# Kernel optimization log

Measured on AMD Instinct MI355X. Metric: run time of the kernel, lower is better.

Reference implementation:

```python
import jax, jax.numpy as jnp
import numpy as np

Q = 8192      # num query tokens
S = 32768     # num support points
E = 131072    # num edges (query<-support neighbor pairs)
D = 256       # token_dim
H = 8         # num_heads
HD = D // H   # head_dim = 32
GEO = 128     # geo mlp_hidden = geo_dim
FFN = 2 * D   # ffn hidden
STAT_IN = 12  # 4 stats * 3 coords
EPS_LN = 1e-5


def gelu(x):
    return jax.nn.gelu(x, approximate=False)  # torch nn.GELU default (erf)


def layernorm(x, g, b):
    m = jnp.mean(x, axis=-1, keepdims=True)
    v = jnp.mean((x - m) ** 2, axis=-1, keepdims=True)
    return (x - m) * jax.lax.rsqrt(v + EPS_LN) * g + b


def setup_inputs() -> dict:
    key = jax.random.key(0)
    ks = jax.random.split(key, 16)
    w = lambda k, shp: jax.random.normal(k, shp, jnp.float32) * 0.02
    return {
        "query_tokens": jax.random.normal(ks[0], (Q, D), jnp.float32),
        "query_pos": jax.random.normal(ks[1], (Q, 3), jnp.float32),
        "support_feats": jax.random.normal(ks[2], (S, D), jnp.float32),
        "support_pos": jax.random.normal(ks[3], (S, 3), jnp.float32),
        "Wq": w(ks[4], (D, D)), "Wk": w(ks[5], (D, D)), "Wv": w(ks[6], (D, D)),
        "Wg": w(ks[7], (GEO, D)),
        "Wo": w(ks[8], (D, D)), "bo": jnp.zeros((D,), jnp.float32),
        "log_tau": jnp.array(0.0, jnp.float32),
        "ln1_g": jnp.ones((D,), jnp.float32), "ln1_b": jnp.zeros((D,), jnp.float32),
        "ln2_g": jnp.ones((D,), jnp.float32), "ln2_b": jnp.zeros((D,), jnp.float32),
        "Wf1": w(ks[9], (D, FFN)), "bf1": jnp.zeros((FFN,), jnp.float32),
        "Wf2": w(ks[10], (FFN, D)), "bf2": jnp.zeros((D,), jnp.float32),
        "Gw1": w(ks[11], (STAT_IN, GEO)), "Gb1": jnp.zeros((GEO,), jnp.float32),
        "Gw2": w(ks[12], (GEO, GEO)), "Gb2": jnp.zeros((GEO,), jnp.float32),
        "q_idx": jnp.sort(jax.random.randint(ks[13], (E,), 0, Q)),
        "s_idx": jax.random.randint(ks[14], (E,), 0, S),
        "num_queries": Q,
    }


def geo_stats(rel, q_idx, num_q):
    # rel: [E,3] relative positions; segmented mean/std/min/max -> [num_q, 12]
    ones = jnp.ones((rel.shape[0], 1), rel.dtype)
    cnt = jnp.maximum(jax.ops.segment_sum(ones, q_idx, num_q), 1.0)  # [Q,1]
    mean = jax.ops.segment_sum(rel, q_idx, num_q) / cnt
    var = jax.ops.segment_sum((rel - mean[q_idx]) ** 2, q_idx, num_q) / cnt
    std = jnp.sqrt(var)
    # torch inits min/max with +/-inf then clamps to [-100,100]; jax segment
    # min/max init with dtype extremes -> same result after clip
    mn = jnp.clip(jax.ops.segment_min(rel, q_idx, num_q), -100.0, 100.0)
    mx = jnp.clip(jax.ops.segment_max(rel, q_idx, num_q), -100.0, 100.0)
    return jnp.concatenate([mean, std, mn, mx], axis=-1)


def reference(query_tokens, query_pos, support_feats, support_pos,
              Wq, Wk, Wv, Wg, Wo, bo, log_tau,
              ln1_g, ln1_b, ln2_g, ln2_b,
              Wf1, bf1, Wf2, bf2, Gw1, Gb1, Gw2, Gb2,
              q_idx, s_idx, num_queries):
    num_q = num_queries
    # ---- statistical geo embedding ----
    rel = support_pos[s_idx] - query_pos[q_idx]                 # [E,3]
    raw = geo_stats(rel, q_idx, num_q)                          # [Q,12]
    geo = gelu(gelu(raw @ Gw1 + Gb1) @ Gw2 + Gb2)               # [Q,GEO]

    # ---- AGNO cross attention (pre-norm) ----
    qt = layernorm(query_tokens, ln1_g, ln1_b)
    Qf = qt @ Wq                                                # [Q,D]
    Kf = support_feats @ Wk                                     # [S,D]
    Vf = support_feats @ Wv                                     # [S,D]
    Gf = geo @ Wg                                               # [Q,D]
    qh = Qf[q_idx].reshape(E, H, HD)
    kh = Kf[s_idx].reshape(E, H, HD)
    vh = Vf[s_idx].reshape(E, H, HD)
    gh = Gf[q_idx].reshape(E, H, HD)
    tau = jnp.exp(log_tau)
    scores = jnp.sum(qh * kh, axis=-1) / (jnp.sqrt(jnp.float32(HD)) * tau)  # [E,H]
    # torch scores_max starts at 0 -> max(0, segment max)
    smax = jnp.maximum(jax.ops.segment_max(scores, q_idx, num_q), 0.0)
    ex = jnp.exp(scores - smax[q_idx])
    ssum = jax.ops.segment_sum(ex, q_idx, num_q)
    alpha = ex / jnp.maximum(ssum[q_idx], 1e-8)                 # [E,H]
    weighted = alpha[..., None] * (vh + gh)                     # [E,H,HD]
    out = jax.ops.segment_sum(weighted, q_idx, num_q)           # [Q,H,HD]
    attn = out.reshape(num_q, D) @ Wo + bo

    # ---- residual + FFN ----
    x = query_tokens + attn
    x = x + gelu(layernorm(x, ln2_g, ln2_b) @ Wf1 + bf1) @ Wf2 + bf2
    return x
```

## Files before the change

### kernel.cpp

```cpp
#include <hip/hip_runtime.h>
#include <math.h>

#define QN 8192
#define SN 32768
#define EN 131072
#define DN 256
#define HN 8
#define HDN 32
#define GEON 128
#define FFNN 512

typedef __attribute__((ext_vector_type(8))) short bf16x8;
typedef __attribute__((ext_vector_type(8))) unsigned short u16x8;
typedef __attribute__((ext_vector_type(4))) unsigned short u16x4;
typedef __attribute__((ext_vector_type(4))) float f32x4;

__device__ __forceinline__ unsigned short f2b(float f) {
  union { float f; unsigned u; } v; v.f = f;
  unsigned u = v.u;
  u += 0x7fffu + ((u >> 16) & 1u);
  return (unsigned short)(u >> 16);
}
__device__ __forceinline__ float b2f(unsigned short h) {
  union { unsigned u; float f; } v; v.u = ((unsigned)h) << 16; return v.f;
}
__device__ __forceinline__ float gelu_f(float x) {
  return 0.5f * x * (1.0f + erff(x * 0.70710678118654752440f));
}

__global__ __launch_bounds__(256) void transpose_weights(
    const float* Wq, const float* Wk, const float* Wv, const float* Wg,
    const float* Wo, const float* Wf1, const float* Wf2,
    unsigned short* WqT, unsigned short* WkvT, unsigned short* WgT,
    unsigned short* WoT, unsigned short* Wf1T, unsigned short* Wf2T) {
  int b = blockIdx.x;
  const float* src; unsigned short* dst; int K, N, tile;
  if (b < 16)       { src = Wq;  dst = WqT;          K = 256; N = 256; tile = b; }
  else if (b < 32)  { src = Wk;  dst = WkvT;         K = 256; N = 256; tile = b - 16; }
  else if (b < 48)  { src = Wv;  dst = WkvT + 65536; K = 256; N = 256; tile = b - 32; }
  else if (b < 56)  { src = Wg;  dst = WgT;          K = 128; N = 256; tile = b - 48; }
  else if (b < 72)  { src = Wo;  dst = WoT;          K = 256; N = 256; tile = b - 56; }
  else if (b < 104) { src = Wf1; dst = Wf1T;         K = 256; N = 512; tile = b - 72; }
  else              { src = Wf2; dst = Wf2T;         K = 512; N = 256; tile = b - 104; }
  int ktiles = K >> 6;
  int k0 = (tile % ktiles) * 64, n0 = (tile / ktiles) * 64;
  __shared__ float ts[64][65];
  int t = threadIdx.x;
  int c4 = (t & 15) * 4;
  int r = t >> 4;
#pragma unroll
  for (int p = 0; p < 4; ++p) {
    int row = p * 16 + r;
    float4 v = *(const float4*)(src + (size_t)(k0 + row) * N + n0 + c4);
    ts[row][c4 + 0] = v.x; ts[row][c4 + 1] = v.y;
    ts[row][c4 + 2] = v.z; ts[row][c4 + 3] = v.w;
  }
  __syncthreads();
#pragma unroll
  for (int p = 0; p < 4; ++p) {
    int n = p * 16 + r;
    ushort4 o;
    o.x = f2b(ts[c4 + 0][n]); o.y = f2b(ts[c4 + 1][n]);
    o.z = f2b(ts[c4 + 2][n]); o.w = f2b(ts[c4 + 3][n]);
    *(ushort4*)(dst + (size_t)(n0 + n) * K + k0 + c4) = o;
  }
}

__global__ __launch_bounds__(256) void seg_offsets(const int* q_idx, int* offs) {
  int i = blockIdx.x * 256 + threadIdx.x;
  if (i > QN) return;
  int lo = 0, hi = EN;
  while (lo < hi) {
    int mid = (lo + hi) >> 1;
    if (q_idx[mid] < i) lo = mid + 1; else hi = mid;
  }
  offs[i] = lo;
}

__global__ __launch_bounds__(256) void geo_stats_kernel(
    const float* qpos, const float* spos, const int* offs, const int* s_idx, float* raw) {
  int q = blockIdx.x * 64 + (threadIdx.x >> 2);
  int sub = threadIdx.x & 3;
  int e0 = offs[q], e1 = offs[q + 1];
  float qx = qpos[q * 3 + 0], qy = qpos[q * 3 + 1], qz = qpos[q * 3 + 2];
  float cnt = 0.f, sx = 0.f, sy = 0.f, sz = 0.f, sxx = 0.f, syy = 0.f, szz = 0.f;
  float mnx = 1e30f, mny = 1e30f, mnz = 1e30f, mxx = -1e30f, mxy = -1e30f, mxz = -1e30f;
  for (int e = e0 + sub; e < e1; e += 4) {
    int s = s_idx[e];
    float rx = spos[s * 3 + 0] - qx;
    float ry = spos[s * 3 + 1] - qy;
    float rz = spos[s * 3 + 2] - qz;
    cnt += 1.f;
    sx += rx; sy += ry; sz += rz;
    sxx += rx * rx; syy += ry * ry; szz += rz * rz;
    mnx = fminf(mnx, rx); mny = fminf(mny, ry); mnz = fminf(mnz, rz);
    mxx = fmaxf(mxx, rx); mxy = fmaxf(mxy, ry); mxz = fmaxf(mxz, rz);
  }
#pragma unroll
  for (int msk = 1; msk <= 2; msk <<= 1) {
    cnt += __shfl_xor(cnt, msk);
    sx += __shfl_xor(sx, msk); sy += __shfl_xor(sy, msk); sz += __shfl_xor(sz, msk);
    sxx += __shfl_xor(sxx, msk); syy += __shfl_xor(syy, msk); szz += __shfl_xor(szz, msk);
    mnx = fminf(mnx, __shfl_xor(mnx, msk));
    mny = fminf(mny, __shfl_xor(mny, msk));
    mnz = fminf(mnz, __shfl_xor(mnz, msk));
    mxx = fmaxf(mxx, __shfl_xor(mxx, msk));
    mxy = fmaxf(mxy, __shfl_xor(mxy, msk));
    mxz = fmaxf(mxz, __shfl_xor(mxz, msk));
  }
  if (sub == 0) {
    float c = fmaxf(cnt, 1.f);
    float mx_ = sx / c, my_ = sy / c, mz_ = sz / c;
    float vx = fmaxf(sxx / c - mx_ * mx_, 0.f);
    float vy = fmaxf(syy / c - my_ * my_, 0.f);
    float vz = fmaxf(szz / c - mz_ * mz_, 0.f);
    float* r = raw + (size_t)q * 12;
    r[0] = mx_; r[1] = my_; r[2] = mz_;
    r[3] = sqrtf(vx); r[4] = sqrtf(vy); r[5] = sqrtf(vz);
    r[6] = fminf(fmaxf(mnx, -100.f), 100.f);
    r[7] = fminf(fmaxf(mny, -100.f), 100.f);
    r[8] = fminf(fmaxf(mnz, -100.f), 100.f);
    r[9] = fminf(fmaxf(mxx, -100.f), 100.f);
    r[10] = fminf(fmaxf(mxy, -100.f), 100.f);
    r[11] = fminf(fmaxf(mxz, -100.f), 100.f);
  }
}

__global__ __launch_bounds__(128) void geo_mlp_kernel(
    const float* raw, const float* Gw1, const float* Gb1,
    const float* Gw2, const float* Gb2, unsigned short* geo_b) {
  int qb = blockIdx.x * 8;
  int j = threadIdx.x;
  __shared__ float rs[8][12];
  __shared__ float h1[8][128];
  if (j < 96) rs[j / 12][j % 12] = raw[(size_t)(qb + j / 12) * 12 + (j % 12)];
  __syncthreads();
  float b1 = Gb1[j];
  float acc[8];
#pragma unroll
  for (int qq = 0; qq < 8; ++qq) acc[qq] = b1;
  for (int i = 0; i < 12; ++i) {
    float w = Gw1[i * GEON + j];
#pragma unroll
    for (int qq = 0; qq < 8; ++qq) acc[qq] += rs[qq][i] * w;
  }
#pragma unroll
  for (int qq = 0; qq < 8; ++qq) h1[qq][j] = gelu_f(acc[qq]);
  __syncthreads();
  float b2 = Gb2[j];
  float acc2[8];
#pragma unroll
  for (int qq = 0; qq < 8; ++qq) acc2[qq] = b2;
  for (int k = 0; k < 128; ++k) {
    float w = Gw2[k * GEON + j];
#pragma unroll
    for (int qq = 0; qq < 8; ++qq) acc2[qq] += h1[qq][k] * w;
  }
#pragma unroll
  for (int qq = 0; qq < 8; ++qq)
    geo_b[(size_t)(qb + qq) * GEON + j] = f2b(gelu_f(acc2[qq]));
}

__global__ __launch_bounds__(256) void ln_kernel(
    const float* x, const float* g, const float* b, unsigned short* out) {
  int row = blockIdx.x * 4 + (threadIdx.x >> 6);
  int lane = threadIdx.x & 63;
  const float* xr = x + (size_t)row * DN;
  float4 v = *(const float4*)(xr + lane * 4);
  float s = v.x + v.y + v.z + v.w;
  float ss = v.x * v.x + v.y * v.y + v.z * v.z + v.w * v.w;
#pragma unroll
  for (int msk = 1; msk <= 32; msk <<= 1) {
    s += __shfl_xor(s, msk);
    ss += __shfl_xor(ss, msk);
  }
  float mean = s * (1.f / 256.f);
  float var = ss * (1.f / 256.f) - mean * mean;
  float rs = 1.0f / sqrtf(var + 1e-5f);
  float4 gg = *(const float4*)(g + lane * 4);
  float4 bb = *(const float4*)(b + lane * 4);
  unsigned short* o = out + (size_t)row * DN + lane * 4;
  o[0] = f2b((v.x - mean) * rs * gg.x + bb.x);
  o[1] = f2b((v.y - mean) * rs * gg.y + bb.y);
  o[2] = f2b((v.z - mean) * rs * gg.z + bb.z);
  o[3] = f2b((v.w - mean) * rs * gg.w + bb.w);
}

__device__ __forceinline__ u16x8* lds_g(unsigned short* base, int row, int col) {
  int g = (col >> 3) ^ (row & 7);
  return reinterpret_cast<u16x8*>(base + row * 256 + g * 8);
}
__global__ __launch_bounds__(256) void kv_gemm(
    const float* A, const unsigned short* BT, unsigned short* KVb) {
  __shared__ unsigned short As[64 * 256];
  __shared__ unsigned short Bs[32 * 256];
  int t = threadIdx.x;
  int bm = blockIdx.x * 64;
  int w = t >> 6, lane = t & 63;
  int quad = lane >> 4, l16 = lane & 15;
  int wr = w >> 1, wc = w & 1;
  int srow = t >> 2, sub = t & 3;
  {
    const float* Ag = A + (size_t)(bm + srow) * 256 + sub * 64;
#pragma unroll
    for (int i = 0; i < 8; ++i) {
      float4 f0 = *(const float4*)(Ag + i * 8);
      float4 f1 = *(const float4*)(Ag + i * 8 + 4);
      u16x8 u;
      u[0] = f2b(f0.x); u[1] = f2b(f0.y); u[2] = f2b(f0.z); u[3] = f2b(f0.w);
      u[4] = f2b(f1.x); u[5] = f2b(f1.y); u[6] = f2b(f1.z); u[7] = f2b(f1.w);
      *lds_g(As, srow, sub * 64 + i * 8) = u;
    }
  }
  int brow = t >> 3, bsub = t & 7;
  for (int ct = 0; ct < 16; ++ct) {
    {
      const unsigned short* Bg = BT + (size_t)(ct * 32 + brow) * 256 + bsub * 32;
#pragma unroll
      for (int i = 0; i < 4; ++i)
        *lds_g(Bs, brow, bsub * 32 + i * 8) = *reinterpret_cast<const u16x8*>(Bg + i * 8);
    }
    __syncthreads();
    f32x4 acc[2];
    acc[0] = (f32x4){0.f, 0.f, 0.f, 0.f};
    acc[1] = (f32x4){0.f, 0.f, 0.f, 0.f};
#pragma unroll
    for (int k = 0; k < 8; ++k) {
      bf16x8 a0 = *reinterpret_cast<bf16x8*>(lds_g(As, wr * 32 + l16, k * 32 + quad * 8));
      bf16x8 a1 = *reinterpret_cast<bf16x8*>(lds_g(As, wr * 32 + 16 + l16, k * 32 + quad * 8));
      bf16x8 b0 = *reinterpret_cast<bf16x8*>(lds_g(Bs, wc * 16 + l16, k * 32 + quad * 8));
      acc[0] = __builtin_amdgcn_mfma_f32_16x16x32_bf16(a0, b0, acc[0], 0, 0, 0);
      acc[1] = __builtin_amdgcn_mfma_f32_16x16x32_bf16(a1, b0, acc[1], 0, 0, 0);
    }
#pragma unroll
    for (int i = 0; i < 2; ++i)
#pragma unroll
      for (int r = 0; r < 4; ++r) {
        int rw = bm + wr * 32 + i * 16 + quad * 4 + r;
        int col = ct * 32 + wc * 16 + l16;
        KVb[(size_t)rw * 512 + col] = f2b(acc[i][r]);
      }
    __syncthreads();
  }
}

template <bool A_FP32, bool COLGRID, bool HAS_BIAS, bool DO_GELU, bool HAS_RESID, bool STORE_F32>
__global__ __launch_bounds__(256) void gemm64(
    const void* Ap, const unsigned short* BT, int M, int N, int K,
    const float* bias, const float* resid, float* outF, unsigned short* outB) {
  __shared__ unsigned short As[64][40];
  __shared__ unsigned short Bs[64][40];
  int t = threadIdx.x;
  int bm = (COLGRID ? blockIdx.x : blockIdx.y) * 64;
  int bn = (COLGRID ? blockIdx.y : blockIdx.x) * 64;
  int w = t >> 6, lane = t & 63;
  int wr = w >> 1, wc = w & 1;
  int quad = lane >> 4, l16 = lane & 15;
  int row = t >> 2, chunk = t & 3;

  f32x4 acc[2][2];
#pragma unroll
  for (int i = 0; i < 2; ++i)
#pragma unroll
    for (int j = 0; j < 2; ++j) acc[i][j] = (f32x4){0.f, 0.f, 0.f, 0.f};

  for (int k0 = 0; k0 < K; k0 += 32) {
    if (A_FP32) {
      const float* Ag = (const float*)Ap + (size_t)(bm + row) * K + k0 + chunk * 8;
      float4 f0 = *(const float4*)Ag;
      float4 f1 = *(const float4*)(Ag + 4);
      u16x8 u;
      u[0] = f2b(f0.x); u[1] = f2b(f0.y); u[2] = f2b(f0.z); u[3] = f2b(f0.w);
      u[4] = f2b(f1.x); u[5] = f2b(f1.y); u[6] = f2b(f1.z); u[7] = f2b(f1.w);
      *reinterpret_cast<u16x8*>(&As[row][chunk * 8]) = u;
    } else {
      const unsigned short* Ag = (const unsigned short*)Ap + (size_t)(bm + row) * K + k0 + chunk * 8;
      *reinterpret_cast<u16x8*>(&As[row][chunk * 8]) = *reinterpret_cast<const u16x8*>(Ag);
    }
    {
      const unsigned short* Bg = BT + (size_t)(bn + row) * K + k0 + chunk * 8;
      *reinterpret_cast<u16x8*>(&Bs[row][chunk * 8]) = *reinterpret_cast<const u16x8*>(Bg);
    }
    __syncthreads();
    bf16x8 a0 = *reinterpret_cast<const bf16x8*>(&As[wr * 32 + l16][quad * 8]);
    bf16x8 a1 = *reinterpret_cast<const bf16x8*>(&As[wr * 32 + 16 + l16][quad * 8]);
    bf16x8 b0 = *reinterpret_cast<const bf16x8*>(&Bs[wc * 32 + l16][quad * 8]);
    bf16x8 b1 = *reinterpret_cast<const bf16x8*>(&Bs[wc * 32 + 16 + l16][quad * 8]);
    acc[0][0] = __builtin_amdgcn_mfma_f32_16x16x32_bf16(a0, b0, acc[0][0], 0, 0, 0);
    acc[0][1] = __builtin_amdgcn_mfma_f32_16x16x32_bf16(a0, b1, acc[0][1], 0, 0, 0);
    acc[1][0] = __builtin_amdgcn_mfma_f32_16x16x32_bf16(a1, b0, acc[1][0], 0, 0, 0);
    acc[1][1] = __builtin_amdgcn_mfma_f32_16x16x32_bf16(a1, b1, acc[1][1], 0, 0, 0);
    __syncthreads();
  }

#pragma unroll
  for (int i = 0; i < 2; ++i)
#pragma unroll
    for (int j = 0; j < 2; ++j) {
      int col = bn + wc * 32 + j * 16 + l16;
      float bv = HAS_BIAS ? bias[col] : 0.f;
#pragma unroll
      for (int r = 0; r < 4; ++r) {
        int rw = bm + wr * 32 + i * 16 + quad * 4 + r;
        float v = acc[i][j][r] + bv;
        if (DO_GELU) v = gelu_f(v);
        if (HAS_RESID) v += resid[(size_t)rw * N + col];
        if (STORE_F32) outF[(size_t)rw * N + col] = v;
        else outB[(size_t)rw * N + col] = f2b(v);
      }
    }
}

__global__ __launch_bounds__(256) void attn_edge_kernel(
    const unsigned short* Qb, const unsigned short* Gfb, const unsigned short* KVb,
    const int* s_idx, const int* offs, const float* log_tau, unsigned short* attn_b) {
  int q = blockIdx.x * 4 + (threadIdx.x >> 6);
  int lane = threadIdx.x & 63;
  int half = lane >> 5;
  int sl = lane & 31;
  int d0 = sl * 8;
  int e0 = offs[q], e1 = offs[q + 1];
  float invs = expf(-log_tau[0]) * 0.17677669529663687f;
  u16x8 qu = *(const u16x8*)(Qb + (size_t)q * DN + d0);
  u16x8 gu = *(const u16x8*)(Gfb + (size_t)q * DN + d0);
  float qf[8], gf[8];
#pragma unroll
  for (int j = 0; j < 8; ++j) { qf[j] = b2f(qu[j]) * invs; gf[j] = b2f(gu[j]); }
  const float NEG = -1e30f;
  float m = -INFINITY, l = 0.f;
  float a[8];
#pragma unroll
  for (int j = 0; j < 8; ++j) a[j] = 0.f;
  for (int e = e0; e < e1; e += 2) {
    int ee = e + half;
    bool valid = ee < e1;
    int s = s_idx[valid ? ee : (e1 - 1)];
    const unsigned short* kr = KVb + (size_t)s * 512 + d0;
    u16x8 ku = *(const u16x8*)kr;
    u16x8 vu = *(const u16x8*)(kr + 256);
    float p = 0.f;
#pragma unroll
    for (int j = 0; j < 8; ++j) p += qf[j] * b2f(ku[j]);
    p += __shfl_xor(p, 1);
    p += __shfl_xor(p, 2);
    if (!valid) p = -INFINITY;
    float mnew = fmaxf(m, p);
    float sc = (m > NEG) ? __expf(m - mnew) : 0.f;
    float we = valid ? __expf(p - mnew) : 0.f;
    l = l * sc + we;
#pragma unroll
    for (int j = 0; j < 8; ++j) a[j] = a[j] * sc + we * (b2f(vu[j]) + gf[j]);
    m = mnew;
  }
  float om = __shfl_xor(m, 32);
  float ol = __shfl_xor(l, 32);
  float M2 = fmaxf(m, om);
  float ws = (m > NEG) ? __expf(m - M2) : 0.f;
  float wo = (om > NEG) ? __expf(om - M2) : 0.f;
  l = l * ws + ol * wo;
#pragma unroll
  for (int j = 0; j < 8; ++j) {
    float oa = __shfl_xor(a[j], 32);
    a[j] = a[j] * ws + oa * wo;
  }
  float M = fmaxf(M2, 0.f);
  float em = (M2 > NEG) ? __expf(M2 - M) : 0.f;
  float denom = fmaxf(l * em, 1e-8f);
  float f = em / denom;
  if (half == 0) {
    u16x8 o;
#pragma unroll
    for (int j = 0; j < 8; ++j) o[j] = f2b(a[j] * f);
    *(u16x8*)(attn_b + (size_t)q * DN + d0) = o;
  }
}

extern "C" void kernel_launch(void* const* d_in, const int* in_sizes, int n_in,
                              void* d_out, int out_size, void* d_ws, size_t ws_size,
                              hipStream_t stream) {
  const float* query_tokens  = (const float*)d_in[0];
  const float* query_pos     = (const float*)d_in[1];
  const float* support_feats = (const float*)d_in[2];
  const float* support_pos   = (const float*)d_in[3];
  const float* Wq  = (const float*)d_in[4];
  const float* Wk  = (const float*)d_in[5];
  const float* Wv  = (const float*)d_in[6];
  const float* Wg  = (const float*)d_in[7];
  const float* Wo  = (const float*)d_in[8];
  const float* bo  = (const float*)d_in[9];
  const float* log_tau = (const float*)d_in[10];
  const float* ln1_g = (const float*)d_in[11];
  const float* ln1_b = (const float*)d_in[12];
  const float* ln2_g = (const float*)d_in[13];
  const float* ln2_b = (const float*)d_in[14];
  const float* Wf1 = (const float*)d_in[15];
  const float* bf1 = (const float*)d_in[16];
  const float* Wf2 = (const float*)d_in[17];
  const float* bf2 = (const float*)d_in[18];
  const float* Gw1 = (const float*)d_in[19];
  const float* Gb1 = (const float*)d_in[20];
  const float* Gw2 = (const float*)d_in[21];
  const float* Gb2 = (const float*)d_in[22];
  const int* q_idx = (const int*)d_in[23];
  const int* s_idx = (const int*)d_in[24];
  float* out = (float*)d_out;

  char* ws = (char*)d_ws;
  size_t off = 0;
  auto alloc = [&](size_t bytes) -> void* {
    void* p = ws + off;
    off = (off + bytes + 255) & ~(size_t)255;
    return p;
  };
  unsigned short* WqT  = (unsigned short*)alloc(65536 * 2);
  unsigned short* WkvT = (unsigned short*)alloc(131072 * 2);
  unsigned short* WgT  = (unsigned short*)alloc(32768 * 2);
  unsigned short* WoT  = (unsigned short*)alloc(65536 * 2);
  unsigned short* Wf1T = (unsigned short*)alloc(131072 * 2);
  unsigned short* Wf2T = (unsigned short*)alloc(131072 * 2);
  int* offs            = (int*)alloc((QN + 1) * 4);
  float* raw           = (float*)alloc((size_t)QN * 12 * 4);
  unsigned short* geo_b = (unsigned short*)alloc((size_t)QN * GEON * 2);
  unsigned short* qt_b  = (unsigned short*)alloc((size_t)QN * DN * 2);
  unsigned short* Qb    = (unsigned short*)alloc((size_t)QN * DN * 2);
  unsigned short* Gf_b  = (unsigned short*)alloc((size_t)QN * DN * 2);
  unsigned short* KVb   = (unsigned short*)alloc((size_t)SN * 512 * 2);
  unsigned short* attn_b = (unsigned short*)alloc((size_t)QN * DN * 2);
  float* x1             = (float*)alloc((size_t)QN * DN * 4);
  unsigned short* z_b   = (unsigned short*)alloc((size_t)QN * DN * 2);
  unsigned short* h_b   = (unsigned short*)alloc((size_t)QN * FFNN * 2);

  transpose_weights<<<136, 256, 0, stream>>>(Wq, Wk, Wv, Wg, Wo, Wf1, Wf2,
                                             WqT, WkvT, WgT, WoT, Wf1T, Wf2T);
  seg_offsets<<<33, 256, 0, stream>>>(q_idx, offs);
  geo_stats_kernel<<<QN / 64, 256, 0, stream>>>(query_pos, support_pos, offs, s_idx, raw);
  geo_mlp_kernel<<<QN / 8, 128, 0, stream>>>(raw, Gw1, Gb1, Gw2, Gb2, geo_b);
  ln_kernel<<<QN / 4, 256, 0, stream>>>(query_tokens, ln1_g, ln1_b, qt_b);
  kv_gemm<<<SN / 64, 256, 0, stream>>>(support_feats, WkvT, KVb);
  gemm64<false, true, false, false, false, false><<<dim3(QN / 64, DN / 64), 256, 0, stream>>>(
      qt_b, WqT, QN, DN, 256, nullptr, nullptr, nullptr, Qb);
  gemm64<false, true, false, false, false, false><<<dim3(QN / 64, DN / 64), 256, 0, stream>>>(
      geo_b, WgT, QN, DN, 128, nullptr, nullptr, nullptr, Gf_b);
  attn_edge_kernel<<<QN / 4, 256, 0, stream>>>(Qb, Gf_b, KVb, s_idx, offs, log_tau, attn_b);
  gemm64<false, true, true, false, true, true><<<dim3(QN / 64, DN / 64), 256, 0, stream>>>(
      attn_b, WoT, QN, DN, 256, bo, query_tokens, x1, nullptr);
  ln_kernel<<<QN / 4, 256, 0, stream>>>(x1, ln2_g, ln2_b, z_b);
  gemm64<false, true, true, true, false, false><<<dim3(QN / 64, FFNN / 64), 256, 0, stream>>>(
      z_b, Wf1T, QN, FFNN, 256, bf1, nullptr, nullptr, h_b);
  gemm64<false, true, true, false, true, true><<<dim3(QN / 64, DN / 64), 256, 0, stream>>>(
      h_b, Wf2T, QN, DN, 512, bf2, x1, out, nullptr);

  (void)in_sizes; (void)n_in; (void)out_size; (void)ws_size;
}
```

Baseline: 252.9 us.

## Fuse LayerNorms into full-K panel GEMMs and prefetch KV weight tiles

Removes both standalone LayerNorm kernels by computing row statistics inside a new single-panel GEMM that loads the whole K extent into LDS, and moves the Q, G, Wo and Wf1 GEMMs onto this panel kernel. kv_gemm now prefetches the next B tile into registers while the current tile is used in MFMAs. The attention kernel stops adding gf to every edge's value and instead adds gf scaled by the normalized softmax mass once at output. These changes cut kernel launches, intermediate bf16 round trips and per-edge ALU work. In exchange the panel kernel uses large LDS buffers, and the LN fusion recomputes the row statistics in every N-column block.

```diff
diff --git a/kernel.cpp b/kernel.cpp
--- a/kernel.cpp
+++ b/kernel.cpp
@@ -26,6 +26,12 @@
 }
 __device__ __forceinline__ float gelu_f(float x) {
   return 0.5f * x * (1.0f + erff(x * 0.70710678118654752440f));
+}
+
+template <int KT>
+__device__ __forceinline__ u16x8* lds_gk(unsigned short* base, int row, int col) {
+  int g = (col >> 3) ^ (row & 7);
+  return reinterpret_cast<u16x8*>(base + row * KT + g * 8);
 }
 
 __global__ __launch_bounds__(256) void transpose_weights(
@@ -161,35 +167,6 @@
     geo_b[(size_t)(qb + qq) * GEON + j] = f2b(gelu_f(acc2[qq]));
 }
 
-__global__ __launch_bounds__(256) void ln_kernel(
-    const float* x, const float* g, const float* b, unsigned short* out) {
-  int row = blockIdx.x * 4 + (threadIdx.x >> 6);
-  int lane = threadIdx.x & 63;
-  const float* xr = x + (size_t)row * DN;
-  float4 v = *(const float4*)(xr + lane * 4);
-  float s = v.x + v.y + v.z + v.w;
-  float ss = v.x * v.x + v.y * v.y + v.z * v.z + v.w * v.w;
-#pragma unroll
-  for (int msk = 1; msk <= 32; msk <<= 1) {
-    s += __shfl_xor(s, msk);
-    ss += __shfl_xor(ss, msk);
-  }
-  float mean = s * (1.f / 256.f);
-  float var = ss * (1.f / 256.f) - mean * mean;
-  float rs = 1.0f / sqrtf(var + 1e-5f);
-  float4 gg = *(const float4*)(g + lane * 4);
-  float4 bb = *(const float4*)(b + lane * 4);
-  unsigned short* o = out + (size_t)row * DN + lane * 4;
-  o[0] = f2b((v.x - mean) * rs * gg.x + bb.x);
-  o[1] = f2b((v.y - mean) * rs * gg.y + bb.y);
-  o[2] = f2b((v.z - mean) * rs * gg.z + bb.z);
-  o[3] = f2b((v.w - mean) * rs * gg.w + bb.w);
-}
-
-__device__ __forceinline__ u16x8* lds_g(unsigned short* base, int row, int col) {
-  int g = (col >> 3) ^ (row & 7);
-  return reinterpret_cast<u16x8*>(base + row * 256 + g * 8);
-}
 __global__ __launch_bounds__(256) void kv_gemm(
     const float* A, const unsigned short* BT, unsigned short* KVb) {
   __shared__ unsigned short As[64 * 256];
@@ -209,26 +186,34 @@
       u16x8 u;
       u[0] = f2b(f0.x); u[1] = f2b(f0.y); u[2] = f2b(f0.z); u[3] = f2b(f0.w);
       u[4] = f2b(f1.x); u[5] = f2b(f1.y); u[6] = f2b(f1.z); u[7] = f2b(f1.w);
-      *lds_g(As, srow, sub * 64 + i * 8) = u;
+      *lds_gk<256>(As, srow, sub * 64 + i * 8) = u;
     }
   }
   int brow = t >> 3, bsub = t & 7;
+  u16x8 pre[4];
+  {
+    const unsigned short* Bg = BT + (size_t)brow * 256 + bsub * 32;
+#pragma unroll
+    for (int i = 0; i < 4; ++i) pre[i] = *reinterpret_cast<const u16x8*>(Bg + i * 8);
+  }
   for (int ct = 0; ct < 16; ++ct) {
-    {
-      const unsigned short* Bg = BT + (size_t)(ct * 32 + brow) * 256 + bsub * 32;
-#pragma unroll
-      for (int i = 0; i < 4; ++i)
-        *lds_g(Bs, brow, bsub * 32 + i * 8) = *reinterpret_cast<const u16x8*>(Bg + i * 8);
-    }
+#pragma unroll
+    for (int i = 0; i < 4; ++i)
+      *lds_gk<256>(Bs, brow, bsub * 32 + i * 8) = pre[i];
     __syncthreads();
+    if (ct < 15) {
+      const unsigned short* Bg = BT + (size_t)((ct + 1) * 32 + brow) * 256 + bsub * 32;
+#pragma unroll
+      for (int i = 0; i < 4; ++i) pre[i] = *reinterpret_cast<const u16x8*>(Bg + i * 8);
+    }
     f32x4 acc[2];
     acc[0] = (f32x4){0.f, 0.f, 0.f, 0.f};
     acc[1] = (f32x4){0.f, 0.f, 0.f, 0.f};
 #pragma unroll
     for (int k = 0; k < 8; ++k) {
-      bf16x8 a0 = *reinterpret_cast<bf16x8*>(lds_g(As, wr * 32 + l16, k * 32 + quad * 8));
-      bf16x8 a1 = *reinterpret_cast<bf16x8*>(lds_g(As, wr * 32 + 16 + l16, k * 32 + quad * 8));
-      bf16x8 b0 = *reinterpret_cast<bf16x8*>(lds_g(Bs, wc * 16 + l16, k * 32 + quad * 8));
+      bf16x8 a0 = *reinterpret_cast<bf16x8*>(lds_gk<256>(As, wr * 32 + l16, k * 32 + quad * 8));
+      bf16x8 a1 = *reinterpret_cast<bf16x8*>(lds_gk<256>(As, wr * 32 + 16 + l16, k * 32 + quad * 8));
+      bf16x8 b0 = *reinterpret_cast<bf16x8*>(lds_gk<256>(Bs, wc * 16 + l16, k * 32 + quad * 8));
       acc[0] = __builtin_amdgcn_mfma_f32_16x16x32_bf16(a0, b0, acc[0], 0, 0, 0);
       acc[1] = __builtin_amdgcn_mfma_f32_16x16x32_bf16(a1, b0, acc[1], 0, 0, 0);
     }
@@ -242,6 +227,106 @@
       }
     __syncthreads();
   }
+}
+
+template <int KT, int AMODE, bool HAS_BIAS, bool DO_GELU, bool HAS_RESID, bool STORE_F32>
+__global__ __launch_bounds__(256) void gemm_panel(
+    const void* Ap, const unsigned short* BT, int N,
+    const float* lng, const float* lnb,
+    const float* bias, const float* resid, float* outF, unsigned short* outB) {
+  __shared__ unsigned short As[64 * KT];
+  __shared__ unsigned short Bs[64 * KT];
+  int t = threadIdx.x;
+  int bm = blockIdx.x * 64, bn = blockIdx.y * 64;
+  int row = t >> 2, sub = t & 3;
+  constexpr int CH = KT / 4;
+
+  if constexpr (AMODE == 1) {
+    static_assert(KT == 256, "LN fusion assumes D=256 rows");
+    const float* Ag = (const float*)Ap + (size_t)(bm + row) * 256 + sub * 64;
+    float va[64];
+    float s = 0.f, ss = 0.f;
+#pragma unroll
+    for (int i = 0; i < 16; ++i) {
+      float4 v = *(const float4*)(Ag + i * 4);
+      va[i * 4 + 0] = v.x; va[i * 4 + 1] = v.y;
+      va[i * 4 + 2] = v.z; va[i * 4 + 3] = v.w;
+      s += v.x + v.y + v.z + v.w;
+      ss += v.x * v.x + v.y * v.y + v.z * v.z + v.w * v.w;
+    }
+    s += __shfl_xor(s, 1);  s += __shfl_xor(s, 2);
+    ss += __shfl_xor(ss, 1); ss += __shfl_xor(ss, 2);
+    float mean = s * (1.f / 256.f);
+    float var = ss * (1.f / 256.f) - mean * mean;
+    float rstd = 1.0f / sqrtf(var + 1e-5f);
+#pragma unroll
+    for (int i = 0; i < 8; ++i) {
+      int c0 = sub * 64 + i * 8;
+      float4 g0 = *(const float4*)(lng + c0);
+      float4 g1 = *(const float4*)(lng + c0 + 4);
+      float4 b0 = *(const float4*)(lnb + c0);
+      float4 b1 = *(const float4*)(lnb + c0 + 4);
+      u16x8 u;
+      u[0] = f2b((va[i * 8 + 0] - mean) * rstd * g0.x + b0.x);
+      u[1] = f2b((va[i * 8 + 1] - mean) * rstd * g0.y + b0.y);
+      u[2] = f2b((va[i * 8 + 2] - mean) * rstd * g0.z + b0.z);
+      u[3] = f2b((va[i * 8 + 3] - mean) * rstd * g0.w + b0.w);
+      u[4] = f2b((va[i * 8 + 4] - mean) * rstd * g1.x + b1.x);
+      u[5] = f2b((va[i * 8 + 5] - mean) * rstd * g1.y + b1.y);
+      u[6] = f2b((va[i * 8 + 6] - mean) * rstd * g1.z + b1.z);
+      u[7] = f2b((va[i * 8 + 7] - mean) * rstd * g1.w + b1.w);
+      *lds_gk<256>(As, row, c0) = u;
+    }
+  } else {
+    const unsigned short* Ag = (const unsigned short*)Ap + (size_t)(bm + row) * KT + sub * CH;
+#pragma unroll
+    for (int i = 0; i < CH / 8; ++i)
+      *lds_gk<KT>(As, row, sub * CH + i * 8) = *reinterpret_cast<const u16x8*>(Ag + i * 8);
+  }
+  {
+    const unsigned short* Bg = BT + (size_t)(bn + row) * KT + sub * CH;
+#pragma unroll
+    for (int i = 0; i < CH / 8; ++i)
+      *lds_gk<KT>(Bs, row, sub * CH + i * 8) = *reinterpret_cast<const u16x8*>(Bg + i * 8);
+  }
+  __syncthreads();
+
+  int w = t >> 6, lane = t & 63;
+  int wr = w >> 1, wc = w & 1;
+  int quad = lane >> 4, l16 = lane & 15;
+  f32x4 acc[2][2];
+#pragma unroll
+  for (int i = 0; i < 2; ++i)
+#pragma unroll
+    for (int j = 0; j < 2; ++j) acc[i][j] = (f32x4){0.f, 0.f, 0.f, 0.f};
+#pragma unroll
+  for (int k = 0; k < KT / 32; ++k) {
+    bf16x8 a0 = *reinterpret_cast<bf16x8*>(lds_gk<KT>(As, wr * 32 + l16, k * 32 + quad * 8));
+    bf16x8 a1 = *reinterpret_cast<bf16x8*>(lds_gk<KT>(As, wr * 32 + 16 + l16, k * 32 + quad * 8));
+    bf16x8 b0 = *reinterpret_cast<bf16x8*>(lds_gk<KT>(Bs, wc * 32 + l16, k * 32 + quad * 8));
+    bf16x8 b1 = *reinterpret_cast<bf16x8*>(lds_gk<KT>(Bs, wc * 32 + 16 + l16, k * 32 + quad * 8));
+    acc[0][0] = __builtin_amdgcn_mfma_f32_16x16x32_bf16(a0, b0, acc[0][0], 0, 0, 0);
+    acc[0][1] = __builtin_amdgcn_mfma_f32_16x16x32_bf16(a0, b1, acc[0][1], 0, 0, 0);
+    acc[1][0] = __builtin_amdgcn_mfma_f32_16x16x32_bf16(a1, b0, acc[1][0], 0, 0, 0);
+    acc[1][1] = __builtin_amdgcn_mfma_f32_16x16x32_bf16(a1, b1, acc[1][1], 0, 0, 0);
+  }
+
+#pragma unroll
+  for (int i = 0; i < 2; ++i)
+#pragma unroll
+    for (int j = 0; j < 2; ++j) {
+      int col = bn + wc * 32 + j * 16 + l16;
+      float bv = HAS_BIAS ? bias[col] : 0.f;
+#pragma unroll
+      for (int r = 0; r < 4; ++r) {
+        int rw = bm + wr * 32 + i * 16 + quad * 4 + r;
+        float v = acc[i][j][r] + bv;
+        if (DO_GELU) v = gelu_f(v);
+        if (HAS_RESID) v += resid[(size_t)rw * N + col];
+        if (STORE_F32) outF[(size_t)rw * N + col] = v;
+        else outB[(size_t)rw * N + col] = f2b(v);
+      }
+    }
 }
 
 template <bool A_FP32, bool COLGRID, bool HAS_BIAS, bool DO_GELU, bool HAS_RESID, bool STORE_F32>
@@ -349,7 +434,7 @@
     float we = valid ? __expf(p - mnew) : 0.f;
     l = l * sc + we;
 #pragma unroll
-    for (int j = 0; j < 8; ++j) a[j] = a[j] * sc + we * (b2f(vu[j]) + gf[j]);
+    for (int j = 0; j < 8; ++j) a[j] = a[j] * sc + we * b2f(vu[j]);
     m = mnew;
   }
   float om = __shfl_xor(m, 32);
@@ -367,10 +452,11 @@
   float em = (M2 > NEG) ? __expf(M2 - M) : 0.f;
   float denom = fmaxf(l * em, 1e-8f);
   float f = em / denom;
+  float sa = l * f;
   if (half == 0) {
     u16x8 o;
 #pragma unroll
-    for (int j = 0; j < 8; ++j) o[j] = f2b(a[j] * f);
+    for (int j = 0; j < 8; ++j) o[j] = f2b(a[j] * f + gf[j] * sa);
     *(u16x8*)(attn_b + (size_t)q * DN + d0) = o;
   }
 }
@@ -421,13 +507,11 @@
   int* offs            = (int*)alloc((QN + 1) * 4);
   float* raw           = (float*)alloc((size_t)QN * 12 * 4);
   unsigned short* geo_b = (unsigned short*)alloc((size_t)QN * GEON * 2);
-  unsigned short* qt_b  = (unsigned short*)alloc((size_t)QN * DN * 2);
   unsigned short* Qb    = (unsigned short*)alloc((size_t)QN * DN * 2);
   unsigned short* Gf_b  = (unsigned short*)alloc((size_t)QN * DN * 2);
   unsigned short* KVb   = (unsigned short*)alloc((size_t)SN * 512 * 2);
   unsigned short* attn_b = (unsigned short*)alloc((size_t)QN * DN * 2);
   float* x1             = (float*)alloc((size_t)QN * DN * 4);
-  unsigned short* z_b   = (unsigned short*)alloc((size_t)QN * DN * 2);
   unsigned short* h_b   = (unsigned short*)alloc((size_t)QN * FFNN * 2);
 
   transpose_weights<<<136, 256, 0, stream>>>(Wq, Wk, Wv, Wg, Wo, Wf1, Wf2,
@@ -435,18 +519,16 @@
   seg_offsets<<<33, 256, 0, stream>>>(q_idx, offs);
   geo_stats_kernel<<<QN / 64, 256, 0, stream>>>(query_pos, support_pos, offs, s_idx, raw);
   geo_mlp_kernel<<<QN / 8, 128, 0, stream>>>(raw, Gw1, Gb1, Gw2, Gb2, geo_b);
-  ln_kernel<<<QN / 4, 256, 0, stream>>>(query_tokens, ln1_g, ln1_b, qt_b);
   kv_gemm<<<SN / 64, 256, 0, stream>>>(support_feats, WkvT, KVb);
-  gemm64<false, true, false, false, false, false><<<dim3(QN / 64, DN / 64), 256, 0, stream>>>(
-      qt_b, WqT, QN, DN, 256, nullptr, nullptr, nullptr, Qb);
-  gemm64<false, true, false, false, false, false><<<dim3(QN / 64, DN / 64), 256, 0, stream>>>(
-      geo_b, WgT, QN, DN, 128, nullptr, nullptr, nullptr, Gf_b);
+  gemm_panel<256, 1, false, false, false, false><<<dim3(QN / 64, 4), 256, 0, stream>>>(
+      query_tokens, WqT, DN, ln1_g, ln1_b, nullptr, nullptr, nullptr, Qb);
+  gemm_panel<128, 0, false, false, false, false><<<dim3(QN / 64, 4), 256, 0, stream>>>(
+      geo_b, WgT, DN, nullptr, nullptr, nullptr, nullptr, nullptr, Gf_b);
   attn_edge_kernel<<<QN / 4, 256, 0, stream>>>(Qb, Gf_b, KVb, s_idx, offs, log_tau, attn_b);
-  gemm64<false, true, true, false, true, true><<<dim3(QN / 64, DN / 64), 256, 0, stream>>>(
-      attn_b, WoT, QN, DN, 256, bo, query_tokens, x1, nullptr);
-  ln_kernel<<<QN / 4, 256, 0, stream>>>(x1, ln2_g, ln2_b, z_b);
-  gemm64<false, true, true, true, false, false><<<dim3(QN / 64, FFNN / 64), 256, 0, stream>>>(
-      z_b, Wf1T, QN, FFNN, 256, bf1, nullptr, nullptr, h_b);
+  gemm_panel<256, 0, true, false, true, true><<<dim3(QN / 64, 4), 256, 0, stream>>>(
+      attn_b, WoT, DN, nullptr, nullptr, bo, query_tokens, x1, nullptr);
+  gemm_panel<256, 1, true, true, false, false><<<dim3(QN / 64, 8), 256, 0, stream>>>(
+      x1, Wf1T, FFNN, ln2_g, ln2_b, bf1, nullptr, nullptr, h_b);
   gemm64<false, true, true, false, true, true><<<dim3(QN / 64, DN / 64), 256, 0, stream>>>(
       h_b, Wf2T, QN, DN, 512, bf2, x1, out, nullptr);
 
```

After: 276.0 us. 1.09x slower.

## Prefetch GEMM tiles into registers and process four edges per wave in attention

Applied to the files above, without the earlier changes.

Both the kv_gemm and generic gemm64 kernels now load the next K/B tile from global memory into registers before the MFMA loop runs on the current tile. The goal is to overlap global-load latency with compute. The attention edge kernel now has each wave process four edges at a time with 16-wide dims per lane instead of two edges with 8-wide dims, which halves the shuffle-reduction depth per dot product. The geometric term is also pulled out of the per-edge accumulate and added once at the end, scaled by the normalized weight sum. These changes raise register pressure and make the final merge across slots more complex.

```diff
diff --git a/kernel.cpp b/kernel.cpp
--- a/kernel.cpp
+++ b/kernel.cpp
@@ -26,6 +26,12 @@
 }
 __device__ __forceinline__ float gelu_f(float x) {
   return 0.5f * x * (1.0f + erff(x * 0.70710678118654752440f));
+}
+
+template <int KT>
+__device__ __forceinline__ u16x8* lds_gk(unsigned short* base, int row, int col) {
+  int g = (col >> 3) ^ (row & 7);
+  return reinterpret_cast<u16x8*>(base + row * KT + g * 8);
 }
 
 __global__ __launch_bounds__(256) void transpose_weights(
@@ -186,10 +192,6 @@
   o[3] = f2b((v.w - mean) * rs * gg.w + bb.w);
 }
 
-__device__ __forceinline__ u16x8* lds_g(unsigned short* base, int row, int col) {
-  int g = (col >> 3) ^ (row & 7);
-  return reinterpret_cast<u16x8*>(base + row * 256 + g * 8);
-}
 __global__ __launch_bounds__(256) void kv_gemm(
     const float* A, const unsigned short* BT, unsigned short* KVb) {
   __shared__ unsigned short As[64 * 256];
@@ -209,26 +211,34 @@
       u16x8 u;
       u[0] = f2b(f0.x); u[1] = f2b(f0.y); u[2] = f2b(f0.z); u[3] = f2b(f0.w);
       u[4] = f2b(f1.x); u[5] = f2b(f1.y); u[6] = f2b(f1.z); u[7] = f2b(f1.w);
-      *lds_g(As, srow, sub * 64 + i * 8) = u;
+      *lds_gk<256>(As, srow, sub * 64 + i * 8) = u;
     }
   }
   int brow = t >> 3, bsub = t & 7;
+  u16x8 pre[4];
+  {
+    const unsigned short* Bg = BT + (size_t)brow * 256 + bsub * 32;
+#pragma unroll
+    for (int i = 0; i < 4; ++i) pre[i] = *reinterpret_cast<const u16x8*>(Bg + i * 8);
+  }
   for (int ct = 0; ct < 16; ++ct) {
-    {
-      const unsigned short* Bg = BT + (size_t)(ct * 32 + brow) * 256 + bsub * 32;
-#pragma unroll
-      for (int i = 0; i < 4; ++i)
-        *lds_g(Bs, brow, bsub * 32 + i * 8) = *reinterpret_cast<const u16x8*>(Bg + i * 8);
-    }
+#pragma unroll
+    for (int i = 0; i < 4; ++i)
+      *lds_gk<256>(Bs, brow, bsub * 32 + i * 8) = pre[i];
     __syncthreads();
+    if (ct < 15) {
+      const unsigned short* Bg = BT + (size_t)((ct + 1) * 32 + brow) * 256 + bsub * 32;
+#pragma unroll
+      for (int i = 0; i < 4; ++i) pre[i] = *reinterpret_cast<const u16x8*>(Bg + i * 8);
+    }
     f32x4 acc[2];
     acc[0] = (f32x4){0.f, 0.f, 0.f, 0.f};
     acc[1] = (f32x4){0.f, 0.f, 0.f, 0.f};
 #pragma unroll
     for (int k = 0; k < 8; ++k) {
-      bf16x8 a0 = *reinterpret_cast<bf16x8*>(lds_g(As, wr * 32 + l16, k * 32 + quad * 8));
-      bf16x8 a1 = *reinterpret_cast<bf16x8*>(lds_g(As, wr * 32 + 16 + l16, k * 32 + quad * 8));
-      bf16x8 b0 = *reinterpret_cast<bf16x8*>(lds_g(Bs, wc * 16 + l16, k * 32 + quad * 8));
+      bf16x8 a0 = *reinterpret_cast<bf16x8*>(lds_gk<256>(As, wr * 32 + l16, k * 32 + quad * 8));
+      bf16x8 a1 = *reinterpret_cast<bf16x8*>(lds_gk<256>(As, wr * 32 + 16 + l16, k * 32 + quad * 8));
+      bf16x8 b0 = *reinterpret_cast<bf16x8*>(lds_gk<256>(Bs, wc * 16 + l16, k * 32 + quad * 8));
       acc[0] = __builtin_amdgcn_mfma_f32_16x16x32_bf16(a0, b0, acc[0], 0, 0, 0);
       acc[1] = __builtin_amdgcn_mfma_f32_16x16x32_bf16(a1, b0, acc[1], 0, 0, 0);
     }
@@ -258,6 +268,16 @@
   int quad = lane >> 4, l16 = lane & 15;
   int row = t >> 2, chunk = t & 3;
 
+  const float* AgF = (const float*)Ap + (size_t)(bm + row) * K + chunk * 8;
+  const unsigned short* AgB = (const unsigned short*)Ap + (size_t)(bm + row) * K + chunk * 8;
+  const unsigned short* Bg = BT + (size_t)(bn + row) * K + chunk * 8;
+
+  float4 pf0, pf1;
+  u16x8 pa, pb;
+  if (A_FP32) { pf0 = *(const float4*)AgF; pf1 = *(const float4*)(AgF + 4); }
+  else        { pa = *(const u16x8*)AgB; }
+  pb = *(const u16x8*)Bg;
+
   f32x4 acc[2][2];
 #pragma unroll
   for (int i = 0; i < 2; ++i)
@@ -265,23 +285,21 @@
     for (int j = 0; j < 2; ++j) acc[i][j] = (f32x4){0.f, 0.f, 0.f, 0.f};
 
   for (int k0 = 0; k0 < K; k0 += 32) {
+    u16x8 ua;
     if (A_FP32) {
-      const float* Ag = (const float*)Ap + (size_t)(bm + row) * K + k0 + chunk * 8;
-      float4 f0 = *(const float4*)Ag;
-      float4 f1 = *(const float4*)(Ag + 4);
-      u16x8 u;
-      u[0] = f2b(f0.x); u[1] = f2b(f0.y); u[2] = f2b(f0.z); u[3] = f2b(f0.w);
-      u[4] = f2b(f1.x); u[5] = f2b(f1.y); u[6] = f2b(f1.z); u[7] = f2b(f1.w);
-      *reinterpret_cast<u16x8*>(&As[row][chunk * 8]) = u;
+      ua[0] = f2b(pf0.x); ua[1] = f2b(pf0.y); ua[2] = f2b(pf0.z); ua[3] = f2b(pf0.w);
+      ua[4] = f2b(pf1.x); ua[5] = f2b(pf1.y); ua[6] = f2b(pf1.z); ua[7] = f2b(pf1.w);
     } else {
-      const unsigned short* Ag = (const unsigned short*)Ap + (size_t)(bm + row) * K + k0 + chunk * 8;
-      *reinterpret_cast<u16x8*>(&As[row][chunk * 8]) = *reinterpret_cast<const u16x8*>(Ag);
-    }
-    {
-      const unsigned short* Bg = BT + (size_t)(bn + row) * K + k0 + chunk * 8;
-      *reinterpret_cast<u16x8*>(&Bs[row][chunk * 8]) = *reinterpret_cast<const u16x8*>(Bg);
-    }
+      ua = pa;
+    }
+    *reinterpret_cast<u16x8*>(&As[row][chunk * 8]) = ua;
+    *reinterpret_cast<u16x8*>(&Bs[row][chunk * 8]) = pb;
     __syncthreads();
+    if (k0 + 32 < K) {
+      if (A_FP32) { pf0 = *(const float4*)(AgF + k0 + 32); pf1 = *(const float4*)(AgF + k0 + 36); }
+      else        { pa = *(const u16x8*)(AgB + k0 + 32); }
+      pb = *(const u16x8*)(Bg + k0 + 32);
+    }
     bf16x8 a0 = *reinterpret_cast<const bf16x8*>(&As[wr * 32 + l16][quad * 8]);
     bf16x8 a1 = *reinterpret_cast<const bf16x8*>(&As[wr * 32 + 16 + l16][quad * 8]);
     bf16x8 b0 = *reinterpret_cast<const bf16x8*>(&Bs[wc * 32 + l16][quad * 8]);
@@ -316,62 +334,83 @@
     const int* s_idx, const int* offs, const float* log_tau, unsigned short* attn_b) {
   int q = blockIdx.x * 4 + (threadIdx.x >> 6);
   int lane = threadIdx.x & 63;
-  int half = lane >> 5;
-  int sl = lane & 31;
-  int d0 = sl * 8;
+  int slot = lane >> 4;
+  int sl = lane & 15;
+  int d0 = sl * 16;
   int e0 = offs[q], e1 = offs[q + 1];
   float invs = expf(-log_tau[0]) * 0.17677669529663687f;
-  u16x8 qu = *(const u16x8*)(Qb + (size_t)q * DN + d0);
-  u16x8 gu = *(const u16x8*)(Gfb + (size_t)q * DN + d0);
-  float qf[8], gf[8];
-#pragma unroll
-  for (int j = 0; j < 8; ++j) { qf[j] = b2f(qu[j]) * invs; gf[j] = b2f(gu[j]); }
+  u16x8 qu0 = *(const u16x8*)(Qb + (size_t)q * DN + d0);
+  u16x8 qu1 = *(const u16x8*)(Qb + (size_t)q * DN + d0 + 8);
+  u16x8 gu0 = *(const u16x8*)(Gfb + (size_t)q * DN + d0);
+  u16x8 gu1 = *(const u16x8*)(Gfb + (size_t)q * DN + d0 + 8);
+  float qf[16], gf[16];
+#pragma unroll
+  for (int j = 0; j < 8; ++j) {
+    qf[j] = b2f(qu0[j]) * invs; qf[j + 8] = b2f(qu1[j]) * invs;
+    gf[j] = b2f(gu0[j]);        gf[j + 8] = b2f(gu1[j]);
+  }
   const float NEG = -1e30f;
   float m = -INFINITY, l = 0.f;
-  float a[8];
-#pragma unroll
-  for (int j = 0; j < 8; ++j) a[j] = 0.f;
-  for (int e = e0; e < e1; e += 2) {
-    int ee = e + half;
+  float a[16];
+#pragma unroll
+  for (int j = 0; j < 16; ++j) a[j] = 0.f;
+  for (int e = e0; e < e1; e += 4) {
+    int ee = e + slot;
     bool valid = ee < e1;
     int s = s_idx[valid ? ee : (e1 - 1)];
     const unsigned short* kr = KVb + (size_t)s * 512 + d0;
-    u16x8 ku = *(const u16x8*)kr;
-    u16x8 vu = *(const u16x8*)(kr + 256);
+    u16x8 ku0 = *(const u16x8*)kr;
+    u16x8 ku1 = *(const u16x8*)(kr + 8);
+    u16x8 vu0 = *(const u16x8*)(kr + 256);
+    u16x8 vu1 = *(const u16x8*)(kr + 264);
     float p = 0.f;
 #pragma unroll
-    for (int j = 0; j < 8; ++j) p += qf[j] * b2f(ku[j]);
+    for (int j = 0; j < 8; ++j) {
+      p += qf[j] * b2f(ku0[j]);
+      p += qf[j + 8] * b2f(ku1[j]);
+    }
     p += __shfl_xor(p, 1);
-    p += __shfl_xor(p, 2);
     if (!valid) p = -INFINITY;
     float mnew = fmaxf(m, p);
     float sc = (m > NEG) ? __expf(m - mnew) : 0.f;
     float we = valid ? __expf(p - mnew) : 0.f;
     l = l * sc + we;
 #pragma unroll
-    for (int j = 0; j < 8; ++j) a[j] = a[j] * sc + we * (b2f(vu[j]) + gf[j]);
+    for (int j = 0; j < 8; ++j) {
+      a[j] = a[j] * sc + we * b2f(vu0[j]);
+      a[j + 8] = a[j + 8] * sc + we * b2f(vu1[j]);
+    }
     m = mnew;
   }
-  float om = __shfl_xor(m, 32);
-  float ol = __shfl_xor(l, 32);
-  float M2 = fmaxf(m, om);
-  float ws = (m > NEG) ? __expf(m - M2) : 0.f;
-  float wo = (om > NEG) ? __expf(om - M2) : 0.f;
-  l = l * ws + ol * wo;
-#pragma unroll
-  for (int j = 0; j < 8; ++j) {
-    float oa = __shfl_xor(a[j], 32);
-    a[j] = a[j] * ws + oa * wo;
-  }
-  float M = fmaxf(M2, 0.f);
-  float em = (M2 > NEG) ? __expf(M2 - M) : 0.f;
+#pragma unroll
+  for (int msk = 16; msk <= 32; msk <<= 1) {
+    float om = __shfl_xor(m, msk);
+    float ol = __shfl_xor(l, msk);
+    float M2 = fmaxf(m, om);
+    float ws = (m > NEG) ? __expf(m - M2) : 0.f;
+    float wo = (om > NEG) ? __expf(om - M2) : 0.f;
+    l = l * ws + ol * wo;
+#pragma unroll
+    for (int j = 0; j < 16; ++j) {
+      float oa = __shfl_xor(a[j], msk);
+      a[j] = a[j] * ws + oa * wo;
+    }
+    m = M2;
+  }
+  float M = fmaxf(m, 0.f);
+  float em = (m > NEG) ? __expf(m - M) : 0.f;
   float denom = fmaxf(l * em, 1e-8f);
   float f = em / denom;
-  if (half == 0) {
-    u16x8 o;
-#pragma unroll
-    for (int j = 0; j < 8; ++j) o[j] = f2b(a[j] * f);
-    *(u16x8*)(attn_b + (size_t)q * DN + d0) = o;
+  float sa = l * f;
+  if (slot == 0) {
+    u16x8 o0, o1;
+#pragma unroll
+    for (int j = 0; j < 8; ++j) {
+      o0[j] = f2b(a[j] * f + gf[j] * sa);
+      o1[j] = f2b(a[j + 8] * f + gf[j + 8] * sa);
+    }
+    *(u16x8*)(attn_b + (size_t)q * DN + d0) = o0;
+    *(u16x8*)(attn_b + (size_t)q * DN + d0 + 8) = o1;
   }
 }
 
```

After: 247.8 us. 2.0% less time.
